# Kernel tuning notes

Measured on AMD Instinct MI355X. Metric: run time of the kernel, lower is better.

## Reference

```python
import jax, jax.numpy as jnp
import numpy as np

ALPHA = 0.2      # LeakyReLU negative slope
NEG_INF = -9e15  # mask value from the original code

def setup_inputs() -> dict:
    key = jax.random.key(0)
    k1, k2, k3, k4 = jax.random.split(key, 4)
    B, M, F_IN, F_OUT = 16, 2048, 128, 64
    h = jax.random.normal(k1, (B, M, F_IN), dtype=jnp.float32)
    adj = jax.random.randint(k2, (B, M, M), 0, 2, dtype=jnp.int32)
    W = jax.random.normal(k3, (F_IN, F_OUT), dtype=jnp.float32) * 0.1
    a = jax.random.normal(k4, (2 * F_OUT, 1), dtype=jnp.float32) * 0.1
    return {"h": h, "adj": adj, "W": W, "a": a}

def reference(h, adj, W, a):
    # h: [B,M,Fin], adj: [B,M,M], W: [Fin,E], a: [2E,1]
    Wh = jnp.matmul(h, W)                      # [B,M,E]
    E = Wh.shape[-1]
    a1, a2 = a[:E, 0], a[E:, 0]
    # decompose a^T [Wh_i || Wh_j] = (Wh_i . a1) + (Wh_j . a2)
    f1 = Wh @ a1                               # [B,M] (source/query term)
    f2 = Wh @ a2                               # [B,M] (target/key term)
    e = jax.nn.leaky_relu(f1[:, :, None] + f2[:, None, :], negative_slope=ALPHA)  # [B,M,M]
    scores = jnp.where(adj > 0, e, NEG_INF)
    attn = jax.nn.softmax(scores, axis=-1)     # [B,M,M]  (dropout p=0 / eval mode)
    h_prime = jnp.matmul(attn, Wh)             # [B,M,E]
    return jax.nn.elu(h_prime)                 # concat=True branch
```

## Files before the change

kernel.cpp:

```cpp
#include <hip/hip_runtime.h>


#define M_     2048
#define FIN_   128
#define F_     64
#define ALPHA_ 0.2f
#define HS_    132
#define WT_    132

typedef float  float4_ __attribute__((ext_vector_type(4)));
typedef short  short8  __attribute__((ext_vector_type(8)));
typedef int    int4_   __attribute__((ext_vector_type(4)));
typedef unsigned int u32x4 __attribute__((ext_vector_type(4)));
typedef unsigned short u16;
typedef unsigned int   u32;

static __device__ __forceinline__ u32 cvtpk(float lo, float hi) {
    u32 r;
    asm("v_cvt_pk_bf16_f32 %0, %1, %2" : "=v"(r) : "v"(lo), "v"(hi));
    return r;
}

__global__ __launch_bounds__(256, 4) void k_prep(
    const float* __restrict__ h, const float* __restrict__ W,
    const float* __restrict__ a, u16* __restrict__ hbf,
    float* __restrict__ f1all, float* __restrict__ f2all)
{
    __shared__ float a_s[2 * F_];
    __shared__ float wa1[FIN_], wa2[FIN_];
    __shared__ float hs[32 * HS_];

    const int tid = threadIdx.x;
    const u32 bid = blockIdx.x;
    const u32 lg  = (bid & 7) * 128 + (bid >> 3);
    const int b   = lg >> 6;
    const int t   = lg & 63;

    if (tid < 128) a_s[tid] = a[tid];

    const int tok = tid >> 3, f0 = (tid & 7) * 16;
    const float* hp = h + ((size_t)(b * M_ + t * 32 + tok)) * FIN_ + f0;
    float4_ x0 = *(const float4_*)hp;
    float4_ x1 = *(const float4_*)(hp + 4);
    float4_ x2 = *(const float4_*)(hp + 8);
    float4_ x3 = *(const float4_*)(hp + 12);
    __syncthreads();

    if (tid < FIN_) {
        float s1 = 0.f, s2 = 0.f;
#pragma unroll 8
        for (int n = 0; n < F_; ++n) {
            float wv = W[tid * F_ + n];
            s1 += wv * a_s[n];
            s2 += wv * a_s[F_ + n];
        }
        wa1[tid] = s1;
        wa2[tid] = s2;
    }

    float* hr = hs + tok * HS_ + f0;
    *(float4_*)(hr)      = x0;
    *(float4_*)(hr + 4)  = x1;
    *(float4_*)(hr + 8)  = x2;
    *(float4_*)(hr + 12) = x3;
    __syncthreads();

    {
        const int l = tid & 63, lc = l & 15, q = l >> 4;
        const int nt0 = (tid >> 6) * 2;
        u32x4* ob = (u32x4*)hbf + ((size_t)(b * 64 + t)) * 8 * 64;
#pragma unroll
        for (int ni = 0; ni < 2; ++ni) {
            const int nt = nt0 + ni;
            const float* cp = hs + (q * 8) * HS_ + nt * 16 + lc;
            u32x4 wv;
            wv[0] = cvtpk(cp[0 * HS_], cp[1 * HS_]);
            wv[1] = cvtpk(cp[2 * HS_], cp[3 * HS_]);
            wv[2] = cvtpk(cp[4 * HS_], cp[5 * HS_]);
            wv[3] = cvtpk(cp[6 * HS_], cp[7 * HS_]);
            ob[nt * 64 + l] = wv;
        }
    }

    {
        const int r = tid >> 3, k0 = (tid & 7) * 16;
        const float* rp = hs + r * HS_ + k0;
        float s1 = 0.f, s2 = 0.f;
#pragma unroll
        for (int k = 0; k < 16; ++k) {
            s1 += rp[k] * wa1[k0 + k];
            s2 += rp[k] * wa2[k0 + k];
        }
        s1 += __shfl_xor(s1, 1, 64); s2 += __shfl_xor(s2, 1, 64);
        s1 += __shfl_xor(s1, 2, 64); s2 += __shfl_xor(s2, 2, 64);
        s1 += __shfl_xor(s1, 4, 64); s2 += __shfl_xor(s2, 4, 64);
        if ((tid & 7) == 0) {
            f1all[b * M_ + t * 32 + r] = s1;
            f2all[b * M_ + t * 32 + r] = s2;
        }
    }
}

__global__ __launch_bounds__(128, 3) void k_main(
    const int* __restrict__ adj, const u16* __restrict__ hbf,
    const float* __restrict__ f1all, const float* __restrict__ f2all,
    const float* __restrict__ W, float* __restrict__ out)
{
    __shared__ char  dyn[WT_ * 32 * 4];
    __shared__ float dens[32];

    float* f2s  = (float*)dyn;
    float* Tsum = (float*)dyn;

    const int tid  = threadIdx.x;
    const int w    = tid >> 6;
    const int l    = tid & 63;
    const int lc   = l & 15;
    const int quad = l >> 4;

    const u32 bid = blockIdx.x;
    const u32 lg  = (bid & 7) * 128 + (bid >> 3);
    const int b   = lg >> 6;
    const int i0  = (lg & 63) * 32;
    const int rowbase = i0 + w * 16;

    {
        const int o = tid * 16;
        float4_ v0 = *(const float4_*)(f2all + b * M_ + o);
        float4_ v1 = *(const float4_*)(f2all + b * M_ + o + 4);
        float4_ v2 = *(const float4_*)(f2all + b * M_ + o + 8);
        float4_ v3 = *(const float4_*)(f2all + b * M_ + o + 12);
        *(float4_*)(f2s + o)      = v0;
        *(float4_*)(f2s + o + 4)  = v1;
        *(float4_*)(f2s + o + 8)  = v2;
        *(float4_*)(f2s + o + 12) = v3;
    }

    const float f1r = f1all[b * M_ + rowbase + lc];
    const int* aprow = adj + ((size_t)(b * M_ + rowbase + lc)) * M_ + quad * 8;
    const u32x4* hb  = (const u32x4*)hbf + ((size_t)b * 64) * 8 * 64 + l;

    int4_ aP0[4], aP1[4];
#pragma unroll
    for (int i = 0; i < 4; ++i) {
        aP0[i] = *(const int4_*)(aprow + i * 32);
        aP1[i] = *(const int4_*)(aprow + i * 32 + 4);
    }
    u32x4 bbA[8], bbB[8];
#pragma unroll
    for (int nt = 0; nt < 8; ++nt) bbA[nt] = hb[nt * 64];

    __syncthreads();

    float denacc = 0.f;
    float4_ acc[8];
#pragma unroll
    for (int nt = 0; nt < 8; ++nt) acc[nt] = (float4_){0.f, 0.f, 0.f, 0.f};

#define SC(GE, GO, AE, AO, IDX)                                 \
        {                                                       \
            float xe = f1r + (GE); xe = fmaxf(xe, ALPHA_ * xe); \
            float xo = f1r + (GO); xo = fmaxf(xo, ALPHA_ * xo); \
            float ee = ((AE) > 0) ? __expf(xe) : 0.f;           \
            float eo = ((AO) > 0) ? __expf(xo) : 0.f;           \
            u32 pk = cvtpk(ee, eo);                             \
            d += __uint_as_float(pk << 16);                     \
            d += __uint_as_float(pk & 0xFFFF0000u);             \
            pw[IDX] = pk;                                       \
        }

#define STAGE(T, I, BC, BN)                                                   \
    {                                                                         \
        const int tn = ((T) < 63) ? (T) + 1 : 63;                             \
        const int tp = ((T) < 60) ? (T) + 4 : 63;                             \
        _Pragma("unroll")                                                     \
        for (int nt = 0; nt < 8; ++nt) BN[nt] = hb[(tn * 8 + nt) * 64];       \
        float4_ g0 = *(const float4_*)(f2s + (T) * 32 + quad * 8);            \
        float4_ g1 = *(const float4_*)(f2s + (T) * 32 + quad * 8 + 4);        \
        u32x4 pw;                                                             \
        float d = 0.f;                                                        \
        SC(g0[0], g0[1], aP0[I][0], aP0[I][1], 0)                             \
        SC(g0[2], g0[3], aP0[I][2], aP0[I][3], 1)                             \
        SC(g1[0], g1[1], aP1[I][0], aP1[I][1], 2)                             \
        SC(g1[2], g1[3], aP1[I][2], aP1[I][3], 3)                             \
        denacc += d;                                                          \
        const short8 af = __builtin_bit_cast(short8, pw);                     \
        aP0[I] = *(const int4_*)(aprow + tp * 32);                            \
        aP1[I] = *(const int4_*)(aprow + tp * 32 + 4);                        \
        _Pragma("unroll")                                                     \
        for (int nt = 0; nt < 8; ++nt)                                        \
            acc[nt] = __builtin_amdgcn_mfma_f32_16x16x32_bf16(                \
                af, __builtin_bit_cast(short8, BC[nt]), acc[nt], 0, 0, 0);    \
    }

    for (int o = 0; o < 16; ++o) {
        const int t0 = o * 4;
        STAGE(t0 + 0, 0, bbA, bbB)
        STAGE(t0 + 1, 1, bbB, bbA)
        STAGE(t0 + 2, 2, bbA, bbB)
        STAGE(t0 + 3, 3, bbB, bbA)
    }
#undef STAGE
#undef SC

    denacc += __shfl_xor(denacc, 16, 64);
    denacc += __shfl_xor(denacc, 32, 64);
    if (quad == 0) dens[w * 16 + lc] = denacc;
    __syncthreads();

#pragma unroll
    for (int nt = 0; nt < 8; ++nt)
#pragma unroll
        for (int mm = 0; mm < 4; ++mm)
            Tsum[(w * 16 + quad * 4 + mm) * WT_ + nt * 16 + lc] = acc[nt][mm];
    __syncthreads();

#pragma unroll
    for (int rr = 0; rr < 2; ++rr) {
        const int r  = (tid >> 3) + rr * 16;
        const int n0 = (tid & 7) * 8;
        const float den  = dens[r];
        const float rden = (den > 0.f) ? (1.f / den) : 0.f;
        float u[8];
#pragma unroll
        for (int nn = 0; nn < 8; ++nn) u[nn] = 0.f;
#pragma unroll 4
        for (int k = 0; k < FIN_; ++k) {
            const float tv = Tsum[r * WT_ + k];
            float4_ wv0 = *(const float4_*)(W + k * F_ + n0);
            float4_ wv1 = *(const float4_*)(W + k * F_ + n0 + 4);
            u[0] += tv * wv0[0]; u[1] += tv * wv0[1];
            u[2] += tv * wv0[2]; u[3] += tv * wv0[3];
            u[4] += tv * wv1[0]; u[5] += tv * wv1[1];
            u[6] += tv * wv1[2]; u[7] += tv * wv1[3];
        }
        float4_ o0, o1;
#pragma unroll
        for (int nn = 0; nn < 8; ++nn) {
            float hp = u[nn] * rden;
            float o  = hp > 0.f ? hp : expm1f(hp);
            if (nn < 4) o0[nn] = o; else o1[nn - 4] = o;
        }
        float* op = out + ((size_t)(b * M_ + i0 + r)) * F_ + n0;
        *(float4_*)op       = o0;
        *(float4_*)(op + 4) = o1;
    }
}

extern "C" void kernel_launch(void* const* d_in, const int* in_sizes, int n_in,
                              void* d_out, int out_size, void* d_ws, size_t ws_size,
                              hipStream_t stream)
{
    (void)out_size; (void)ws_size;
    const float* h  = (const float*)d_in[0];
    const int* adjp = (const int*)d_in[1];
    const float* Wp = (const float*)d_in[2];
    const float* ap = (const float*)d_in[3];
    for (int i = 0; i < n_in; ++i) {
        long s = in_sizes[i];
        if      (s == 4194304L)  h    = (const float*)d_in[i];
        else if (s == 67108864L) adjp = (const int*)d_in[i];
        else if (s == 8192L)     Wp   = (const float*)d_in[i];
        else if (s == 128L)      ap   = (const float*)d_in[i];
    }
    u16*   hbf   = (u16*)d_ws;
    float* f1all = (float*)((char*)d_ws + (8u << 20));
    float* f2all = f1all + 16 * M_;
    k_prep<<<1024, 256, 0, stream>>>(h, Wp, ap, hbf, f1all, f2all);
    k_main<<<1024, 128, 0, stream>>>(adjp, hbf, f1all, f2all, Wp, (float*)d_out);
}
```

Before: 448.0 us.

## Split key dimension across two wave pairs and use nontemporal adjacency loads

Doubles the block to 256 threads and splits the 2048-column key loop so that each pair of waves covers half of the columns for the same 16-row tiles. The partial accumulators and denominators are combined through shared memory afterwards. Adjacency loads become nontemporal with a shallower prefetch distance. The register double-buffering of hbf tiles is dropped in favour of in-stage loads, which may expose more load latency, and the reduction adds an extra shared-memory pass and a barrier.

```diff
diff --git a/kernel.cpp b/kernel.cpp
--- a/kernel.cpp
+++ b/kernel.cpp
@@ -19,6 +19,10 @@
     u32 r;
     asm("v_cvt_pk_bf16_f32 %0, %1, %2" : "=v"(r) : "v"(lo), "v"(hi));
     return r;
+}
+
+static __device__ __forceinline__ int4_ ntload4(const int* p) {
+    return __builtin_nontemporal_load((const int4_*)p);
 }
 
 __global__ __launch_bounds__(256, 4) void k_prep(
@@ -101,13 +105,13 @@
     }
 }
 
-__global__ __launch_bounds__(128, 3) void k_main(
+__global__ __launch_bounds__(256, 4) void k_main(
     const int* __restrict__ adj, const u16* __restrict__ hbf,
     const float* __restrict__ f1all, const float* __restrict__ f2all,
     const float* __restrict__ W, float* __restrict__ out)
 {
     __shared__ char  dyn[WT_ * 32 * 4];
-    __shared__ float dens[32];
+    __shared__ float dens2[64];
 
     float* f2s  = (float*)dyn;
     float* Tsum = (float*)dyn;
@@ -117,38 +121,34 @@
     const int l    = tid & 63;
     const int lc   = l & 15;
     const int quad = l >> 4;
+    const int wr   = w & 1;
+    const int wh   = w >> 1;
 
     const u32 bid = blockIdx.x;
     const u32 lg  = (bid & 7) * 128 + (bid >> 3);
     const int b   = lg >> 6;
     const int i0  = (lg & 63) * 32;
-    const int rowbase = i0 + w * 16;
-
-    {
-        const int o = tid * 16;
+    const int rowbase = i0 + wr * 16;
+
+    {
+        const int o = tid * 8;
         float4_ v0 = *(const float4_*)(f2all + b * M_ + o);
         float4_ v1 = *(const float4_*)(f2all + b * M_ + o + 4);
-        float4_ v2 = *(const float4_*)(f2all + b * M_ + o + 8);
-        float4_ v3 = *(const float4_*)(f2all + b * M_ + o + 12);
-        *(float4_*)(f2s + o)      = v0;
-        *(float4_*)(f2s + o + 4)  = v1;
-        *(float4_*)(f2s + o + 8)  = v2;
-        *(float4_*)(f2s + o + 12) = v3;
+        *(float4_*)(f2s + o)     = v0;
+        *(float4_*)(f2s + o + 4) = v1;
     }
 
     const float f1r = f1all[b * M_ + rowbase + lc];
     const int* aprow = adj + ((size_t)(b * M_ + rowbase + lc)) * M_ + quad * 8;
     const u32x4* hb  = (const u32x4*)hbf + ((size_t)b * 64) * 8 * 64 + l;
 
-    int4_ aP0[4], aP1[4];
-#pragma unroll
-    for (int i = 0; i < 4; ++i) {
-        aP0[i] = *(const int4_*)(aprow + i * 32);
-        aP1[i] = *(const int4_*)(aprow + i * 32 + 4);
-    }
-    u32x4 bbA[8], bbB[8];
-#pragma unroll
-    for (int nt = 0; nt < 8; ++nt) bbA[nt] = hb[nt * 64];
+    const int t0 = wh * 32;
+    const int tE = t0 + 31;
+
+    int4_ aA0 = ntload4(aprow + t0 * 32);
+    int4_ aA1 = ntload4(aprow + t0 * 32 + 4);
+    int4_ aB0 = ntload4(aprow + (t0 + 1) * 32);
+    int4_ aB1 = ntload4(aprow + (t0 + 1) * 32 + 4);
 
     __syncthreads();
 
@@ -169,57 +169,63 @@
             pw[IDX] = pk;                                       \
         }
 
-#define STAGE(T, I, BC, BN)                                                   \
+#define STAGE(T, A0, A1)                                                      \
     {                                                                         \
-        const int tn = ((T) < 63) ? (T) + 1 : 63;                             \
-        const int tp = ((T) < 60) ? (T) + 4 : 63;                             \
+        const int tp = ((T) + 2 <= tE) ? (T) + 2 : tE;                        \
+        u32x4 bb[8];                                                          \
         _Pragma("unroll")                                                     \
-        for (int nt = 0; nt < 8; ++nt) BN[nt] = hb[(tn * 8 + nt) * 64];       \
+        for (int nt = 0; nt < 8; ++nt) bb[nt] = hb[((T) * 8 + nt) * 64];      \
         float4_ g0 = *(const float4_*)(f2s + (T) * 32 + quad * 8);            \
         float4_ g1 = *(const float4_*)(f2s + (T) * 32 + quad * 8 + 4);        \
         u32x4 pw;                                                             \
         float d = 0.f;                                                        \
-        SC(g0[0], g0[1], aP0[I][0], aP0[I][1], 0)                             \
-        SC(g0[2], g0[3], aP0[I][2], aP0[I][3], 1)                             \
-        SC(g1[0], g1[1], aP1[I][0], aP1[I][1], 2)                             \
-        SC(g1[2], g1[3], aP1[I][2], aP1[I][3], 3)                             \
+        SC(g0[0], g0[1], A0[0], A0[1], 0)                                     \
+        SC(g0[2], g0[3], A0[2], A0[3], 1)                                     \
+        SC(g1[0], g1[1], A1[0], A1[1], 2)                                     \
+        SC(g1[2], g1[3], A1[2], A1[3], 3)                                     \
         denacc += d;                                                          \
         const short8 af = __builtin_bit_cast(short8, pw);                     \
-        aP0[I] = *(const int4_*)(aprow + tp * 32);                            \
-        aP1[I] = *(const int4_*)(aprow + tp * 32 + 4);                        \
+        A0 = ntload4(aprow + tp * 32);                                        \
+        A1 = ntload4(aprow + tp * 32 + 4);                                    \
         _Pragma("unroll")                                                     \
         for (int nt = 0; nt < 8; ++nt)                                        \
             acc[nt] = __builtin_amdgcn_mfma_f32_16x16x32_bf16(                \
-                af, __builtin_bit_cast(short8, BC[nt]), acc[nt], 0, 0, 0);    \
+                af, __builtin_bit_cast(short8, bb[nt]), acc[nt], 0, 0, 0);    \
     }
 
     for (int o = 0; o < 16; ++o) {
-        const int t0 = o * 4;
-        STAGE(t0 + 0, 0, bbA, bbB)
-        STAGE(t0 + 1, 1, bbB, bbA)
-        STAGE(t0 + 2, 2, bbA, bbB)
-        STAGE(t0 + 3, 3, bbB, bbA)
+        STAGE(t0 + 2 * o,     aA0, aA1)
+        STAGE(t0 + 2 * o + 1, aB0, aB1)
     }
 #undef STAGE
 #undef SC
 
     denacc += __shfl_xor(denacc, 16, 64);
     denacc += __shfl_xor(denacc, 32, 64);
-    if (quad == 0) dens[w * 16 + lc] = denacc;
-    __syncthreads();
-
-#pragma unroll
-    for (int nt = 0; nt < 8; ++nt)
-#pragma unroll
-        for (int mm = 0; mm < 4; ++mm)
-            Tsum[(w * 16 + quad * 4 + mm) * WT_ + nt * 16 + lc] = acc[nt][mm];
-    __syncthreads();
-
-#pragma unroll
-    for (int rr = 0; rr < 2; ++rr) {
-        const int r  = (tid >> 3) + rr * 16;
+    if (quad == 0) dens2[wh * 32 + wr * 16 + lc] = denacc;
+    __syncthreads();
+
+    if (wh == 0) {
+#pragma unroll
+        for (int nt = 0; nt < 8; ++nt)
+#pragma unroll
+            for (int mm = 0; mm < 4; ++mm)
+                Tsum[(wr * 16 + quad * 4 + mm) * WT_ + nt * 16 + lc] = acc[nt][mm];
+    }
+    __syncthreads();
+    if (wh == 1) {
+#pragma unroll
+        for (int nt = 0; nt < 8; ++nt)
+#pragma unroll
+            for (int mm = 0; mm < 4; ++mm)
+                Tsum[(wr * 16 + quad * 4 + mm) * WT_ + nt * 16 + lc] += acc[nt][mm];
+    }
+    __syncthreads();
+
+    {
+        const int r  = tid >> 3;
         const int n0 = (tid & 7) * 8;
-        const float den  = dens[r];
+        const float den  = dens2[r] + dens2[32 + r];
         const float rden = (den > 0.f) ? (1.f / den) : 0.f;
         float u[8];
 #pragma unroll
@@ -267,5 +273,5 @@
     float* f1all = (float*)((char*)d_ws + (8u << 20));
     float* f2all = f1all + 16 * M_;
     k_prep<<<1024, 256, 0, stream>>>(h, Wp, ap, hbf, f1all, f2all);
-    k_main<<<1024, 128, 0, stream>>>(adjp, hbf, f1all, f2all, Wp, (float*)d_out);
-}
+    k_main<<<1024, 256, 0, stream>>>(adjp, hbf, f1all, f2all, Wp, (float*)d_out);
+}
```

New measurement: 445.0 us. About the same (-0.7%).
